# Kernel optimization log

Measured on AMD Instinct MI355X. Metric: run time of the kernel, lower is better.

The kernel has to match this reference:

```python
import jax, jax.numpy as jnp
import numpy as np


def causal_fft_conv(v, h):
    # v: [B, L, D], h: [L, D]; causal (linear, not circular) conv via zero-padded FFT
    L = v.shape[1]
    n = 2 * L
    Vf = jnp.fft.rfft(v, n=n, axis=1)          # [B, n//2+1, D]
    Hf = jnp.fft.rfft(h, n=n, axis=0)          # [n//2+1, D]
    y = jnp.fft.irfft(Vf * Hf[None], n=n, axis=1)
    return y[:, :L].astype(v.dtype)


def setup_inputs() -> dict:
    key = jax.random.key(0)
    ks = jax.random.split(key, 5)
    B, L, D = 4, 4096, 1024
    scale = 1.0 / np.sqrt(D)
    x = jax.random.normal(ks[0], (B, L, D), dtype=jnp.float32)
    Wu = jax.random.normal(ks[1], (D, D), dtype=jnp.float32) * scale
    Wv = jax.random.normal(ks[2], (D, D), dtype=jnp.float32) * scale
    Wo = jax.random.normal(ks[3], (D, D), dtype=jnp.float32) * scale
    h_filter = jax.random.normal(ks[4], (L, D), dtype=jnp.float32) * 0.02
    bu = jnp.zeros((D,), jnp.float32)
    bv = jnp.zeros((D,), jnp.float32)
    bo = jnp.zeros((D,), jnp.float32)
    return {"x": x, "Wu": Wu, "bu": bu, "Wv": Wv, "bv": bv,
            "h_filter": h_filter, "Wo": Wo, "bo": bo}


def reference(x, Wu, bu, Wv, bv, h_filter, Wo, bo):
    L = x.shape[1]
    u = jnp.einsum('bld,de->ble', x, Wu) + bu
    v = jnp.einsum('bld,de->ble', x, Wv) + bv
    t = jnp.arange(L, dtype=x.dtype)
    decay = jnp.exp(-0.01 * t)[:, None]          # [L, 1]
    h = h_filter * decay                          # [L, D]
    v_conv = causal_fft_conv(v, h)                # [B, L, D]
    y = u * v_conv
    y = jnp.einsum('bld,de->ble', y, Wo) + bo
    return y
```

## Files before the change

### kernel.cpp

```cpp
#include <hip/hip_runtime.h>
#include <hip/hip_bf16.h>
#include <hip/hip_fp16.h>
#include <string.h>

typedef __hip_bfloat16 bf16;
typedef _Float16 f16;
typedef __attribute__((ext_vector_type(8))) short short8;
typedef __attribute__((ext_vector_type(4))) float floatx4;
typedef __attribute__((ext_vector_type(4))) unsigned int uintx4;

#define GLD16(gp, lp) __builtin_amdgcn_global_load_lds( \
    (__attribute__((address_space(1))) void*)(gp),      \
    (__attribute__((address_space(3))) void*)(lp), 16, 0, 0)

__device__ __forceinline__ unsigned short bf16_bits(float f) {
  bf16 h = (bf16)f;
  unsigned short s;
  memcpy(&s, &h, 2);
  return s;
}
__device__ __forceinline__ __half2 u2h2(unsigned u) {
  __half2 h;
  memcpy(&h, &u, 4);
  return h;
}

__global__ __launch_bounds__(256)
void cvtx_k(const float* __restrict__ x, char* __restrict__ outbase,
            size_t bstride) {
  size_t e = ((size_t)blockIdx.x * 256 + threadIdx.x) * 8;
  int b = (int)(e >> 22);
  size_t i = e & 4194303;
  const floatx4* s = (const floatx4*)(x + e);
  floatx4 a0 = s[0], a1 = s[1];
  union { uintx4 u4; unsigned short us[8]; } w;
  w.us[0] = bf16_bits(a0.x); w.us[1] = bf16_bits(a0.y);
  w.us[2] = bf16_bits(a0.z); w.us[3] = bf16_bits(a0.w);
  w.us[4] = bf16_bits(a1.x); w.us[5] = bf16_bits(a1.y);
  w.us[6] = bf16_bits(a1.z); w.us[7] = bf16_bits(a1.w);
  *(uintx4*)((bf16*)(outbase + (size_t)b * bstride) + i) = w.u4;
}

__global__ __launch_bounds__(256)
void transpose_k(const float* __restrict__ W0, const float* __restrict__ W1,
                 const float* __restrict__ W2, bf16* __restrict__ T0,
                 bf16* __restrict__ T1, bf16* __restrict__ T2) {
  __shared__ bf16 t[64][66];
  const float* S = blockIdx.z == 0 ? W0 : (blockIdx.z == 1 ? W1 : W2);
  bf16* Dst      = blockIdx.z == 0 ? T0 : (blockIdx.z == 1 ? T1 : T2);
  const int tx = threadIdx.x & 63, ty = threadIdx.x >> 6;
  const int kb = blockIdx.y * 64, nb = blockIdx.x * 64;
#pragma unroll
  for (int rr = 0; rr < 16; ++rr) {
    int r = ty * 16 + rr;
    t[r][tx] = (bf16)S[(size_t)(kb + r) * 1024 + nb + tx];
  }
  __syncthreads();
#pragma unroll
  for (int rr = 0; rr < 16; ++rr) {
    int r = ty * 16 + rr;
    Dst[(size_t)(nb + r) * 1024 + kb + tx] = t[tx][r];
  }
}

__global__ __launch_bounds__(256)
void hprep_k(const float* __restrict__ hf, f16* __restrict__ hp) {
  int idx = blockIdx.x * 256 + threadIdx.x;
  int dblk = idx >> 15;
  int rem = idx & 32767;
  int k = rem >> 6, dd = rem & 63;
  int d = dblk * 64 + dd;
  float val = hf[(size_t)k * 1024 + d] * __expf(-0.01f * (float)k);
  hp[idx] = (f16)val;
}

__device__ __forceinline__
void gemm_body256(const bf16* __restrict__ A, const bf16* __restrict__ Bt,
                  const float* __restrict__ bias, void* __restrict__ Cout,
                  int out_mode, int m0, int n0) {
  constexpr int K = 1024;
  __shared__ __align__(16) bf16 Asl[2][16384];
  __shared__ __align__(16) bf16 Bsl[2][16384];
  const int tid = threadIdx.x;
  const int lane = tid & 63;
  const int wave = tid >> 6;
  const int wm = wave >> 2, wn = wave & 3;
  const int r = lane & 15, qlane = lane >> 4;

  floatx4 acc[8][4] = {};

  const bf16* gA[4];
  const bf16* gB[4];
#pragma unroll
  for (int is = 0; is < 4; ++is) {
    int p = is * 512 + tid;
    int m = p >> 3;
    int qe = (p & 7) ^ (m & 7);
    gA[is] = A  + (size_t)(m0 + m) * K + qe * 8;
    gB[is] = Bt + (size_t)(n0 + m) * K + qe * 8;
  }
  const int wbyte = wave * 1024;

  const int rx = r & 7;
  const int aRow = (wm * 128 + r) * 128;
  const int bRow = (wn * 64 + r) * 128;
  const int a0off = aRow + ((qlane) ^ rx) * 16;
  const int a1off = aRow + ((4 + qlane) ^ rx) * 16;
  const int b0off = bRow + ((qlane) ^ rx) * 16;
  const int b1off = bRow + ((4 + qlane) ^ rx) * 16;

#pragma unroll
  for (int is = 0; is < 4; ++is)
    GLD16(gA[is], (char*)&Asl[0][0] + is * 8192 + wbyte);
#pragma unroll
  for (int is = 0; is < 4; ++is)
    GLD16(gB[is], (char*)&Bsl[0][0] + is * 8192 + wbyte);

  for (int kt = 0; kt < 16; ++kt) {
    const int cur = kt & 1;
    const char* Ab = (const char*)&Asl[cur][0];
    const char* Bb = (const char*)&Bsl[cur][0];

    if (kt < 15) {
      const int k0 = (kt + 1) * 64;
#pragma unroll
      for (int is = 0; is < 4; ++is)
        GLD16(gA[is] + k0, (char*)&Asl[cur ^ 1][0] + is * 8192 + wbyte);
#pragma unroll
      for (int is = 0; is < 4; ++is)
        GLD16(gB[is] + k0, (char*)&Bsl[cur ^ 1][0] + is * 8192 + wbyte);
      asm volatile("s_waitcnt vmcnt(8)" ::: "memory");
    } else {
      asm volatile("s_waitcnt vmcnt(0)" ::: "memory");
    }
    __builtin_amdgcn_s_barrier();

    {
      short8 af[8], bfr[4];
#pragma unroll
      for (int i = 0; i < 8; ++i)
        af[i] = *(const short8*)(Ab + a0off + i * 2048);
#pragma unroll
      for (int j = 0; j < 4; ++j)
        bfr[j] = *(const short8*)(Bb + b0off + j * 2048);
      __builtin_amdgcn_s_setprio(1);
#pragma unroll
      for (int i = 0; i < 8; ++i)
#pragma unroll
        for (int j = 0; j < 4; ++j)
          acc[i][j] = __builtin_amdgcn_mfma_f32_16x16x32_bf16(
              af[i], bfr[j], acc[i][j], 0, 0, 0);
      __builtin_amdgcn_s_setprio(0);
    }
    {
      short8 af[8], bfr[4];
#pragma unroll
      for (int i = 0; i < 8; ++i)
        af[i] = *(const short8*)(Ab + a1off + i * 2048);
#pragma unroll
      for (int j = 0; j < 4; ++j)
        bfr[j] = *(const short8*)(Bb + b1off + j * 2048);
      __builtin_amdgcn_s_setprio(1);
#pragma unroll
      for (int i = 0; i < 8; ++i)
#pragma unroll
        for (int j = 0; j < 4; ++j)
          acc[i][j] = __builtin_amdgcn_mfma_f32_16x16x32_bf16(
              af[i], bfr[j], acc[i][j], 0, 0, 0);
      __builtin_amdgcn_s_setprio(0);
    }
    __builtin_amdgcn_s_barrier();
  }

  const int cb = n0 + wn * 64;
  float bvv[4];
#pragma unroll
  for (int j = 0; j < 4; ++j) bvv[j] = bias[cb + j * 16 + r];
#pragma unroll
  for (int i = 0; i < 8; ++i) {
    int rowb = m0 + wm * 128 + i * 16 + qlane * 4;
#pragma unroll
    for (int j = 0; j < 4; ++j) {
      int col = cb + j * 16 + r;
#pragma unroll
      for (int v = 0; v < 4; ++v) {
        float val = acc[i][j][v] + bvv[j];
        size_t off = (size_t)(rowb + v) * 1024 + col;
        if (out_mode == 0)      ((bf16*)Cout)[off] = (bf16)val;
        else if (out_mode == 1) ((f16*)Cout)[off] = (f16)val;
        else                    ((float*)Cout)[off] = val;
      }
    }
  }
}

__global__ __launch_bounds__(512, 2)
void gemm_uv_k(const bf16* __restrict__ A, const bf16* __restrict__ WuT,
               const bf16* __restrict__ WvT, const float* __restrict__ bu,
               const float* __restrict__ bv, bf16* __restrict__ u_out,
               f16* __restrict__ v_out) {
  const int isv = blockIdx.z;
  gemm_body256(A, isv ? WvT : WuT, isv ? bv : bu,
               isv ? (void*)v_out : (void*)u_out, isv,
               blockIdx.x * 256, blockIdx.y * 256);
}

__global__ __launch_bounds__(512, 2)
void gemm_o_k(const bf16* __restrict__ A, const bf16* __restrict__ Bt,
              const float* __restrict__ bias, float* __restrict__ C) {
  gemm_body256(A, Bt, bias, (void*)C, 2, blockIdx.x * 256, blockIdx.y * 256);
}

__global__ __launch_bounds__(256)
void conv_k(const f16* __restrict__ vg0, const f16* __restrict__ hp,
            bf16* __restrict__ up0) {
  constexpr int CC = 64, TT = 128, D = 1024;
  __shared__ __align__(16) unsigned vs2[(TT + CC) * 32];
  __shared__ __align__(16) unsigned hs2[CC * 32];
  const int tid = threadIdx.x;
  const int pp = tid & 31, tg = tid >> 5;
  const int bx = blockIdx.x;
  const int t0 = blockIdx.y * TT;
  const int base = tg * 16;
  const unsigned* vg32 = (const unsigned*)(vg0 + (size_t)blockIdx.z * 4096 * D);
  unsigned* up32 = (unsigned*)(up0 + (size_t)blockIdx.z * 4096 * D);
  const uintx4* vg4 = (const uintx4*)vg32;
  const uintx4* hp4 = (const uintx4*)hp + (size_t)bx * 512 * 8;

  float ax[16], ay[16];
#pragma unroll
  for (int i = 0; i < 16; ++i) { ax[i] = 0.f; ay[i] = 0.f; }

  for (int c = 0; c < 8; ++c) {
    const int k0 = c * CC;
    __syncthreads();
    {
      uintx4* hd = (uintx4*)hs2;
      hd[tid] = hp4[k0 * 8 + tid];
      hd[tid + 256] = hp4[k0 * 8 + tid + 256];
    }
    {
      uintx4* vd = (uintx4*)vs2;
#pragma unroll
      for (int it = 0; it < 6; ++it) {
        int q = it * 256 + tid;
        int row = q >> 3, dp4 = q & 7;
        int tau = t0 - k0 - CC + row;
        uintx4 val = {0, 0, 0, 0};
        if (tau >= 0) val = vg4[(size_t)tau * 128 + bx * 8 + dp4];
        vd[q] = val;
      }
    }
    __syncthreads();

    __half2 p[16];
#pragma unroll
    for (int i = 0; i < 16; ++i)
      p[i] = u2h2(vs2[(base + i + CC) * 32 + pp]);
    __half2 acc2[16];
    const __half2 z2 = __float2half2_rn(0.f);
#pragma unroll
    for (int i = 0; i < 16; ++i) acc2[i] = z2;

    for (int kb = 0; kb < 4; ++kb) {
#pragma unroll
      for (int k2 = 0; k2 < 16; ++k2) {
        const int kk = kb * 16 + k2;
        __half2 hk = u2h2(hs2[kk * 32 + pp]);
#pragma unroll
        for (int i = 0; i < 16; ++i)
          acc2[i] = __hfma2(hk, p[(i - k2) & 15], acc2[i]);
        p[(15 - k2) & 15] = u2h2(vs2[(base + CC - 1 - kk) * 32 + pp]);
      }
    }
#pragma unroll
    for (int i = 0; i < 16; ++i) {
      ax[i] += __low2float(acc2[i]);
      ay[i] += __high2float(acc2[i]);
    }
  }

  const size_t rb = (size_t)(t0 + base) * 512 + bx * 32 + pp;
#pragma unroll
  for (int i = 0; i < 16; ++i) {
    unsigned uw = up32[rb + (size_t)i * 512];
    float ul = __uint_as_float((uw & 0xffffu) << 16);
    float uh = __uint_as_float(uw & 0xffff0000u);
    unsigned lo = bf16_bits(ul * ax[i]);
    unsigned hi = bf16_bits(uh * ay[i]);
    up32[rb + (size_t)i * 512] = lo | (hi << 16);
  }
}

extern "C" void kernel_launch(void* const* d_in, const int* in_sizes, int n_in,
                              void* d_out, int out_size, void* d_ws,
                              size_t ws_size, hipStream_t stream) {
  const float* x  = (const float*)d_in[0];
  const float* Wu = (const float*)d_in[1];
  const float* bu = (const float*)d_in[2];
  const float* Wv = (const float*)d_in[3];
  const float* bv = (const float*)d_in[4];
  const float* hf = (const float*)d_in[5];
  const float* Wo = (const float*)d_in[6];
  const float* bo = (const float*)d_in[7];
  char* ws = (char*)d_ws;
  bf16* WuT = (bf16*)(ws);
  bf16* WvT = (bf16*)(ws + 2097152);
  bf16* WoT = (bf16*)(ws + 4194304);
  f16*  hp  = (f16*)(ws + 6291456);

  dim3 tb(256);
  dim3 tg(512);
  transpose_k<<<dim3(16, 16, 3), tb, 0, stream>>>(Wu, Wv, Wo, WuT, WvT, WoT);
  hprep_k<<<dim3(2048), tb, 0, stream>>>(hf, hp);

  if (ws_size >= 42991616ull) {
    bf16* xb = (bf16*)d_out;
    f16*  vf = (f16*)((char*)d_out + 33554432);
    bf16* u  = (bf16*)(ws + 8388608);
    cvtx_k<<<dim3(8192), tb, 0, stream>>>(x, (char*)d_out, 8388608);
    gemm_uv_k<<<dim3(64, 4, 2), tg, 0, stream>>>(xb, WuT, WvT, bu, bv, u, vf);
    conv_k<<<dim3(16, 32, 4), tb, 0, stream>>>(vf, hp, u);
    gemm_o_k<<<dim3(64, 4), tg, 0, stream>>>(u, WoT, bo, (float*)d_out);
  } else {
    bf16* u_b = (bf16*)(ws + 8388608);
    cvtx_k<<<dim3(8192), tb, 0, stream>>>(x, (char*)d_out, 16777216);
    for (int b = 0; b < 4; ++b) {
      char* quarter = (char*)d_out + (size_t)b * 16777216;
      bf16* xb = (bf16*)quarter;
      f16*  vb = (f16*)(quarter + 8388608);
      float* outb = (float*)d_out + (size_t)b * 4194304;
      gemm_uv_k<<<dim3(16, 4, 2), tg, 0, stream>>>(xb, WuT, WvT, bu, bv,
                                                   u_b, vb);
      conv_k<<<dim3(16, 32, 1), tb, 0, stream>>>(vb, hp, u_b);
      gemm_o_k<<<dim3(16, 4), tg, 0, stream>>>(u_b, WoT, bo, outb);
    }
  }
}
```

Before: 419.2 us.

## Split GEMM k-tile into four quadrant phases with staggered prefetch

Restructures the 256x256 bf16 GEMM main loop so each k-tile is computed in four quadrant sub-phases (A-half x B-half). Global-to-LDS loads for the next tile are issued in pieces between phases, with finer vmcnt waits and barriers. The LDS data layout is remapped so each piece lands in the quadrant it feeds. The aim is to overlap loads with MFMA work and cut register pressure from fragments, in exchange for more barriers and tricky wait-count bookkeeping.

Result: slower. 432.0 us (+3.1%).

```diff
diff --git a/kernel.cpp b/kernel.cpp
--- a/kernel.cpp
+++ b/kernel.cpp
@@ -86,89 +86,156 @@
   const int wave = tid >> 6;
   const int wm = wave >> 2, wn = wave & 3;
   const int r = lane & 15, qlane = lane >> 4;
+  const int rx = r & 7;
+  const int lrow = lane >> 3;
+  const int lq = (lane & 7) ^ lrow;
 
   floatx4 acc[8][4] = {};
 
-  const bf16* gA[4];
-  const bf16* gB[4];
-#pragma unroll
-  for (int is = 0; is < 4; ++is) {
-    int p = is * 512 + tid;
-    int m = p >> 3;
-    int qe = (p & 7) ^ (m & 7);
-    gA[is] = A  + (size_t)(m0 + m) * K + qe * 8;
-    gB[is] = Bt + (size_t)(n0 + m) * K + qe * 8;
-  }
-  const int wbyte = wave * 1024;
-
-  const int rx = r & 7;
-  const int aRow = (wm * 128 + r) * 128;
-  const int bRow = (wn * 64 + r) * 128;
-  const int a0off = aRow + ((qlane) ^ rx) * 16;
-  const int a1off = aRow + ((4 + qlane) ^ rx) * 16;
-  const int b0off = bRow + ((qlane) ^ rx) * 16;
-  const int b1off = bRow + ((4 + qlane) ^ rx) * 16;
-
-#pragma unroll
-  for (int is = 0; is < 4; ++is)
-    GLD16(gA[is], (char*)&Asl[0][0] + is * 8192 + wbyte);
-#pragma unroll
-  for (int is = 0; is < 4; ++is)
-    GLD16(gB[is], (char*)&Bsl[0][0] + is * 8192 + wbyte);
+  const int rho0 = wave * 16, rho1 = rho0 + 8;
+  const int a1g0 = rho0 + (rho0 & 64), a1g1 = rho1 + (rho1 & 64);
+  const int a2g0 = a1g0 + 64,          a2g1 = a1g1 + 64;
+  const int b1g0 = ((rho0 >> 5) << 6) + (rho0 & 31);
+  const int b1g1 = ((rho1 >> 5) << 6) + (rho1 & 31);
+  const int b2g0 = b1g0 + 32,          b2g1 = b1g1 + 32;
+
+  const bf16* Ag = A  + (size_t)m0 * K + lq * 8;
+  const bf16* Bg = Bt + (size_t)n0 * K + lq * 8;
+  const bf16* gA1a = Ag + (size_t)(a1g0 + lrow) * K;
+  const bf16* gA1b = Ag + (size_t)(a1g1 + lrow) * K;
+  const bf16* gA2a = Ag + (size_t)(a2g0 + lrow) * K;
+  const bf16* gA2b = Ag + (size_t)(a2g1 + lrow) * K;
+  const bf16* gB1a = Bg + (size_t)(b1g0 + lrow) * K;
+  const bf16* gB1b = Bg + (size_t)(b1g1 + lrow) * K;
+  const bf16* gB2a = Bg + (size_t)(b2g0 + lrow) * K;
+  const bf16* gB2b = Bg + (size_t)(b2g1 + lrow) * K;
+
+  const int col0 = (qlane ^ rx) * 16;
+  const int col1 = ((4 + qlane) ^ rx) * 16;
+
+  {
+    char* An = (char*)&Asl[0][0];
+    char* Bn = (char*)&Bsl[0][0];
+    GLD16(gA1a, An + a1g0 * 128);
+    GLD16(gA1b, An + a1g1 * 128);
+    GLD16(gA2a, An + a2g0 * 128);
+    GLD16(gA2b, An + a2g1 * 128);
+    GLD16(gB1a, Bn + b1g0 * 128);
+    GLD16(gB1b, Bn + b1g1 * 128);
+    GLD16(gB2a, Bn + b2g0 * 128);
+    GLD16(gB2b, Bn + b2g1 * 128);
+    asm volatile("s_waitcnt vmcnt(0)" ::: "memory");
+    __builtin_amdgcn_s_barrier();
+  }
 
   for (int kt = 0; kt < 16; ++kt) {
-    const int cur = kt & 1;
-    const char* Ab = (const char*)&Asl[cur][0];
-    const char* Bb = (const char*)&Bsl[cur][0];
+    const int s = kt & 1;
+    const char* Ab = (const char*)&Asl[s][0];
+    const char* Bb = (const char*)&Bsl[s][0];
+    char* An = (char*)&Asl[s ^ 1][0];
+    char* Bn = (char*)&Bsl[s ^ 1][0];
+    const int kb = (kt + 1) * 64;
+    const char* Aw0 = Ab + wm * 16384 + r * 128 + col0;
+    const char* Aw1 = Ab + wm * 16384 + r * 128 + col1;
+    const char* Bw0 = Bb + wn * 8192 + r * 128 + col0;
+    const char* Bw1 = Bb + wn * 8192 + r * 128 + col1;
+    short8 af[4][2], bf[2][2];
 
     if (kt < 15) {
-      const int k0 = (kt + 1) * 64;
-#pragma unroll
-      for (int is = 0; is < 4; ++is)
-        GLD16(gA[is] + k0, (char*)&Asl[cur ^ 1][0] + is * 8192 + wbyte);
-#pragma unroll
-      for (int is = 0; is < 4; ++is)
-        GLD16(gB[is] + k0, (char*)&Bsl[cur ^ 1][0] + is * 8192 + wbyte);
-      asm volatile("s_waitcnt vmcnt(8)" ::: "memory");
+      GLD16(gA1a + kb, An + a1g0 * 128);
+      GLD16(gA1b + kb, An + a1g1 * 128);
+      asm volatile("s_waitcnt vmcnt(4)" ::: "memory");
+    } else {
+      asm volatile("s_waitcnt vmcnt(2)" ::: "memory");
+    }
+    __builtin_amdgcn_s_barrier();
+#pragma unroll
+    for (int i = 0; i < 4; ++i) {
+      af[i][0] = *(const short8*)(Aw0 + i * 2048);
+      af[i][1] = *(const short8*)(Aw1 + i * 2048);
+    }
+#pragma unroll
+    for (int j = 0; j < 2; ++j) {
+      bf[j][0] = *(const short8*)(Bw0 + j * 2048);
+      bf[j][1] = *(const short8*)(Bw1 + j * 2048);
+    }
+    __builtin_amdgcn_s_setprio(1);
+#pragma unroll
+    for (int ks = 0; ks < 2; ++ks)
+#pragma unroll
+      for (int i = 0; i < 4; ++i)
+#pragma unroll
+        for (int j = 0; j < 2; ++j)
+          acc[i][j] = __builtin_amdgcn_mfma_f32_16x16x32_bf16(
+              af[i][ks], bf[j][ks], acc[i][j], 0, 0, 0);
+    __builtin_amdgcn_s_setprio(0);
+
+    if (kt < 15) {
+      GLD16(gA2a + kb, An + a2g0 * 128);
+      GLD16(gA2b + kb, An + a2g1 * 128);
+      asm volatile("s_waitcnt vmcnt(4)" ::: "memory");
     } else {
       asm volatile("s_waitcnt vmcnt(0)" ::: "memory");
     }
     __builtin_amdgcn_s_barrier();
-
-    {
-      short8 af[8], bfr[4];
-#pragma unroll
-      for (int i = 0; i < 8; ++i)
-        af[i] = *(const short8*)(Ab + a0off + i * 2048);
-#pragma unroll
-      for (int j = 0; j < 4; ++j)
-        bfr[j] = *(const short8*)(Bb + b0off + j * 2048);
-      __builtin_amdgcn_s_setprio(1);
-#pragma unroll
-      for (int i = 0; i < 8; ++i)
-#pragma unroll
-        for (int j = 0; j < 4; ++j)
-          acc[i][j] = __builtin_amdgcn_mfma_f32_16x16x32_bf16(
-              af[i], bfr[j], acc[i][j], 0, 0, 0);
-      __builtin_amdgcn_s_setprio(0);
-    }
-    {
-      short8 af[8], bfr[4];
-#pragma unroll
-      for (int i = 0; i < 8; ++i)
-        af[i] = *(const short8*)(Ab + a1off + i * 2048);
-#pragma unroll
-      for (int j = 0; j < 4; ++j)
-        bfr[j] = *(const short8*)(Bb + b1off + j * 2048);
-      __builtin_amdgcn_s_setprio(1);
-#pragma unroll
-      for (int i = 0; i < 8; ++i)
-#pragma unroll
-        for (int j = 0; j < 4; ++j)
-          acc[i][j] = __builtin_amdgcn_mfma_f32_16x16x32_bf16(
-              af[i], bfr[j], acc[i][j], 0, 0, 0);
-      __builtin_amdgcn_s_setprio(0);
-    }
+#pragma unroll
+    for (int j = 0; j < 2; ++j) {
+      bf[j][0] = *(const short8*)(Bw0 + (2 + j) * 2048);
+      bf[j][1] = *(const short8*)(Bw1 + (2 + j) * 2048);
+    }
+    __builtin_amdgcn_s_setprio(1);
+#pragma unroll
+    for (int ks = 0; ks < 2; ++ks)
+#pragma unroll
+      for (int i = 0; i < 4; ++i)
+#pragma unroll
+        for (int j = 0; j < 2; ++j)
+          acc[i][2 + j] = __builtin_amdgcn_mfma_f32_16x16x32_bf16(
+              af[i][ks], bf[j][ks], acc[i][2 + j], 0, 0, 0);
+    __builtin_amdgcn_s_setprio(0);
+
+    if (kt < 15) {
+      GLD16(gB1a + kb, Bn + b1g0 * 128);
+      GLD16(gB1b + kb, Bn + b1g1 * 128);
+      asm volatile("s_waitcnt vmcnt(10)" ::: "memory");
+    }
+    __builtin_amdgcn_s_barrier();
+#pragma unroll
+    for (int i = 0; i < 4; ++i) {
+      af[i][0] = *(const short8*)(Aw0 + 8192 + i * 2048);
+      af[i][1] = *(const short8*)(Aw1 + 8192 + i * 2048);
+    }
+    __builtin_amdgcn_s_setprio(1);
+#pragma unroll
+    for (int ks = 0; ks < 2; ++ks)
+#pragma unroll
+      for (int i = 0; i < 4; ++i)
+#pragma unroll
+        for (int j = 0; j < 2; ++j)
+          acc[4 + i][2 + j] = __builtin_amdgcn_mfma_f32_16x16x32_bf16(
+              af[i][ks], bf[j][ks], acc[4 + i][2 + j], 0, 0, 0);
+    __builtin_amdgcn_s_setprio(0);
+
+    if (kt < 15) {
+      GLD16(gB2a + kb, Bn + b2g0 * 128);
+      GLD16(gB2b + kb, Bn + b2g1 * 128);
+    }
+#pragma unroll
+    for (int j = 0; j < 2; ++j) {
+      bf[j][0] = *(const short8*)(Bw0 + j * 2048);
+      bf[j][1] = *(const short8*)(Bw1 + j * 2048);
+    }
+    __builtin_amdgcn_s_setprio(1);
+#pragma unroll
+    for (int ks = 0; ks < 2; ++ks)
+#pragma unroll
+      for (int i = 0; i < 4; ++i)
+#pragma unroll
+        for (int j = 0; j < 2; ++j)
+          acc[4 + i][j] = __builtin_amdgcn_mfma_f32_16x16x32_bf16(
+              af[i][ks], bf[j][ks], acc[4 + i][j], 0, 0, 0);
+    __builtin_amdgcn_s_setprio(0);
+    __builtin_amdgcn_sched_barrier(0);
     __builtin_amdgcn_s_barrier();
   }
 
```

## Restructure GEMM main loop into quadrant-pipelined 8-wave schedule with staggered prefetch

Applied to the files above, without the earlier changes.

The GEMM body now splits each K-tile into four quadrant sub-steps (A-half by B-half). Each sub-step interleaves its LDS fragment reads and half-tile global-to-LDS prefetches with MFMA bursts, separated by barriers and sched_barriers. The aim is to overlap memory traffic with matrix math and cut register pressure by holding only half the fragments at once. The conv loop also software-pipelines its filter-tap LDS loads two steps ahead. The trade-off is many more barriers per K-tile and tricky buffer-reuse ordering, which could stall or race.

New measurement: 438.8 us. 1.05x slower.

```diff
diff --git a/kernel.cpp b/kernel.cpp
--- a/kernel.cpp
+++ b/kernel.cpp
@@ -86,89 +86,168 @@
   const int wave = tid >> 6;
   const int wm = wave >> 2, wn = wave & 3;
   const int r = lane & 15, qlane = lane >> 4;
+  const int rx = r & 7;
+  const int lrow = lane >> 3;
+  const int lgr = (lane & 7) ^ lrow;
 
   floatx4 acc[8][4] = {};
 
-  const bf16* gA[4];
-  const bf16* gB[4];
-#pragma unroll
-  for (int is = 0; is < 4; ++is) {
-    int p = is * 512 + tid;
-    int m = p >> 3;
-    int qe = (p & 7) ^ (m & 7);
-    gA[is] = A  + (size_t)(m0 + m) * K + qe * 8;
-    gB[is] = Bt + (size_t)(n0 + m) * K + qe * 8;
-  }
-  const int wbyte = wave * 1024;
-
-  const int rx = r & 7;
-  const int aRow = (wm * 128 + r) * 128;
-  const int bRow = (wn * 64 + r) * 128;
-  const int a0off = aRow + ((qlane) ^ rx) * 16;
-  const int a1off = aRow + ((4 + qlane) ^ rx) * 16;
-  const int b0off = bRow + ((qlane) ^ rx) * 16;
-  const int b1off = bRow + ((4 + qlane) ^ rx) * 16;
-
-#pragma unroll
-  for (int is = 0; is < 4; ++is)
-    GLD16(gA[is], (char*)&Asl[0][0] + is * 8192 + wbyte);
-#pragma unroll
-  for (int is = 0; is < 4; ++is)
-    GLD16(gB[is], (char*)&Bsl[0][0] + is * 8192 + wbyte);
+  const int a1r0 = wave * 8 + lrow;
+  const int a1r1 = 128 + wave * 8 + lrow;
+  const int a2r0 = a1r0 + 64, a2r1 = a1r1 + 64;
+  const int bL0 = wave * 8 + lrow, bL1 = 64 + wave * 8 + lrow;
+  const int b1r0 = ((bL0 >> 5) << 6) + (bL0 & 31);
+  const int b1r1 = ((bL1 >> 5) << 6) + (bL1 & 31);
+  const int b2r0 = b1r0 + 32, b2r1 = b1r1 + 32;
+
+  const bf16* gA1a = A + (size_t)(m0 + a1r0) * K + lgr * 8;
+  const bf16* gA1b = A + (size_t)(m0 + a1r1) * K + lgr * 8;
+  const bf16* gA2a = A + (size_t)(m0 + a2r0) * K + lgr * 8;
+  const bf16* gA2b = A + (size_t)(m0 + a2r1) * K + lgr * 8;
+  const bf16* gB1a = Bt + (size_t)(n0 + b1r0) * K + lgr * 8;
+  const bf16* gB1b = Bt + (size_t)(n0 + b1r1) * K + lgr * 8;
+  const bf16* gB2a = Bt + (size_t)(n0 + b2r0) * K + lgr * 8;
+  const bf16* gB2b = Bt + (size_t)(n0 + b2r1) * K + lgr * 8;
+
+  const int dA1a = (wave * 8) * 128, dA1b = (128 + wave * 8) * 128;
+  const int dA2a = dA1a + 8192,      dA2b = dA1b + 8192;
+  const int bb0 = ((wave * 8) >> 5) * 64 + ((wave * 8) & 31);
+  const int bb1 = ((64 + wave * 8) >> 5) * 64 + ((64 + wave * 8) & 31);
+  const int dB1a = bb0 * 128, dB1b = bb1 * 128;
+  const int dB2a = dB1a + 4096, dB2b = dB1b + 4096;
+
+  {
+    char* A0 = (char*)&Asl[0][0];
+    char* B0 = (char*)&Bsl[0][0];
+    char* A1p = (char*)&Asl[1][0];
+    char* B1p = (char*)&Bsl[1][0];
+    GLD16(gA1a, A0 + dA1a); GLD16(gA1b, A0 + dA1b);
+    GLD16(gB1a, B0 + dB1a); GLD16(gB1b, B0 + dB1b);
+    GLD16(gB2a, B0 + dB2a); GLD16(gB2b, B0 + dB2b);
+    GLD16(gA2a, A0 + dA2a); GLD16(gA2b, A0 + dA2b);
+    GLD16(gA1a + 64, A1p + dA1a); GLD16(gA1b + 64, A1p + dA1b);
+    GLD16(gB2a + 64, B1p + dB2a); GLD16(gB2b + 64, B1p + dB2b);
+    GLD16(gA2a + 64, A1p + dA2a); GLD16(gA2b + 64, A1p + dA2b);
+    asm volatile("s_waitcnt vmcnt(6)" ::: "memory");
+    __builtin_amdgcn_s_barrier();
+  }
 
   for (int kt = 0; kt < 16; ++kt) {
-    const int cur = kt & 1;
-    const char* Ab = (const char*)&Asl[cur][0];
-    const char* Bb = (const char*)&Bsl[cur][0];
-
+    const int s = kt & 1;
+    const char* Ab = (const char*)&Asl[s][0];
+    const char* Bb = (const char*)&Bsl[s][0];
+    char* Ao = (char*)&Asl[s][0];
+    char* Bo = (char*)&Bsl[s][0];
+    char* Bn = (char*)&Bsl[s ^ 1][0];
+    const int k1 = (kt + 1) * 64, k2o = (kt + 2) * 64;
+    const char* Arow = Ab + (wm * 128 + r) * 128;
+    const char* Brow = Bb + (wn * 64 + r) * 128;
+    const int c0 = (qlane ^ rx) * 16, c1 = ((4 + qlane) ^ rx) * 16;
+    short8 af[4][2], bf[2][2];
+
+#pragma unroll
+    for (int mi = 0; mi < 4; ++mi) {
+      af[mi][0] = *(const short8*)(Arow + mi * 2048 + c0);
+      af[mi][1] = *(const short8*)(Arow + mi * 2048 + c1);
+    }
+#pragma unroll
+    for (int nj = 0; nj < 2; ++nj) {
+      bf[nj][0] = *(const short8*)(Brow + nj * 2048 + c0);
+      bf[nj][1] = *(const short8*)(Brow + nj * 2048 + c1);
+    }
     if (kt < 15) {
-      const int k0 = (kt + 1) * 64;
-#pragma unroll
-      for (int is = 0; is < 4; ++is)
-        GLD16(gA[is] + k0, (char*)&Asl[cur ^ 1][0] + is * 8192 + wbyte);
-#pragma unroll
-      for (int is = 0; is < 4; ++is)
-        GLD16(gB[is] + k0, (char*)&Bsl[cur ^ 1][0] + is * 8192 + wbyte);
-      asm volatile("s_waitcnt vmcnt(8)" ::: "memory");
+      GLD16(gB1a + k1, Bn + dB1a);
+      GLD16(gB1b + k1, Bn + dB1b);
+    }
+    asm volatile("s_waitcnt lgkmcnt(8)" ::: "memory");
+    __builtin_amdgcn_s_barrier();
+    asm volatile("s_waitcnt lgkmcnt(0)" ::: "memory");
+    __builtin_amdgcn_sched_barrier(0);
+    __builtin_amdgcn_s_setprio(1);
+#pragma unroll
+    for (int ks = 0; ks < 2; ++ks)
+#pragma unroll
+      for (int mi = 0; mi < 4; ++mi)
+#pragma unroll
+        for (int nj = 0; nj < 2; ++nj)
+          acc[mi][nj] = __builtin_amdgcn_mfma_f32_16x16x32_bf16(
+              af[mi][ks], bf[nj][ks], acc[mi][nj], 0, 0, 0);
+    __builtin_amdgcn_s_setprio(0);
+    __builtin_amdgcn_s_barrier();
+
+#pragma unroll
+    for (int nj = 0; nj < 2; ++nj) {
+      bf[nj][0] = *(const short8*)(Brow + 4096 + nj * 2048 + c0);
+      bf[nj][1] = *(const short8*)(Brow + 4096 + nj * 2048 + c1);
+    }
+    if (kt < 14) {
+      GLD16(gA1a + k2o, Ao + dA1a);
+      GLD16(gA1b + k2o, Ao + dA1b);
+    }
+    __builtin_amdgcn_s_barrier();
+    asm volatile("s_waitcnt lgkmcnt(0)" ::: "memory");
+    __builtin_amdgcn_sched_barrier(0);
+    __builtin_amdgcn_s_setprio(1);
+#pragma unroll
+    for (int ks = 0; ks < 2; ++ks)
+#pragma unroll
+      for (int mi = 0; mi < 4; ++mi)
+#pragma unroll
+        for (int nj = 0; nj < 2; ++nj)
+          acc[mi][2 + nj] = __builtin_amdgcn_mfma_f32_16x16x32_bf16(
+              af[mi][ks], bf[nj][ks], acc[mi][2 + nj], 0, 0, 0);
+    __builtin_amdgcn_s_setprio(0);
+    __builtin_amdgcn_s_barrier();
+
+#pragma unroll
+    for (int mi = 0; mi < 4; ++mi) {
+      af[mi][0] = *(const short8*)(Arow + 8192 + mi * 2048 + c0);
+      af[mi][1] = *(const short8*)(Arow + 8192 + mi * 2048 + c1);
+    }
+    if (kt < 14) {
+      GLD16(gB2a + k2o, Bo + dB2a);
+      GLD16(gB2b + k2o, Bo + dB2b);
+    }
+    __builtin_amdgcn_s_barrier();
+    asm volatile("s_waitcnt lgkmcnt(0)" ::: "memory");
+    __builtin_amdgcn_sched_barrier(0);
+    __builtin_amdgcn_s_setprio(1);
+#pragma unroll
+    for (int ks = 0; ks < 2; ++ks)
+#pragma unroll
+      for (int mi = 0; mi < 4; ++mi)
+#pragma unroll
+        for (int nj = 0; nj < 2; ++nj)
+          acc[4 + mi][2 + nj] = __builtin_amdgcn_mfma_f32_16x16x32_bf16(
+              af[mi][ks], bf[nj][ks], acc[4 + mi][2 + nj], 0, 0, 0);
+    __builtin_amdgcn_s_setprio(0);
+    __builtin_amdgcn_s_barrier();
+
+#pragma unroll
+    for (int nj = 0; nj < 2; ++nj) {
+      bf[nj][0] = *(const short8*)(Brow + nj * 2048 + c0);
+      bf[nj][1] = *(const short8*)(Brow + nj * 2048 + c1);
+    }
+    if (kt < 14) {
+      GLD16(gA2a + k2o, Ao + dA2a);
+      GLD16(gA2b + k2o, Ao + dA2b);
+      asm volatile("s_waitcnt vmcnt(6)" ::: "memory");
     } else {
       asm volatile("s_waitcnt vmcnt(0)" ::: "memory");
     }
     __builtin_amdgcn_s_barrier();
-
-    {
-      short8 af[8], bfr[4];
-#pragma unroll
-      for (int i = 0; i < 8; ++i)
-        af[i] = *(const short8*)(Ab + a0off + i * 2048);
-#pragma unroll
-      for (int j = 0; j < 4; ++j)
-        bfr[j] = *(const short8*)(Bb + b0off + j * 2048);
-      __builtin_amdgcn_s_setprio(1);
-#pragma unroll
-      for (int i = 0; i < 8; ++i)
-#pragma unroll
-        for (int j = 0; j < 4; ++j)
-          acc[i][j] = __builtin_amdgcn_mfma_f32_16x16x32_bf16(
-              af[i], bfr[j], acc[i][j], 0, 0, 0);
-      __builtin_amdgcn_s_setprio(0);
-    }
-    {
-      short8 af[8], bfr[4];
-#pragma unroll
-      for (int i = 0; i < 8; ++i)
-        af[i] = *(const short8*)(Ab + a1off + i * 2048);
-#pragma unroll
-      for (int j = 0; j < 4; ++j)
-        bfr[j] = *(const short8*)(Bb + b1off + j * 2048);
-      __builtin_amdgcn_s_setprio(1);
-#pragma unroll
-      for (int i = 0; i < 8; ++i)
-#pragma unroll
-        for (int j = 0; j < 4; ++j)
-          acc[i][j] = __builtin_amdgcn_mfma_f32_16x16x32_bf16(
-              af[i], bfr[j], acc[i][j], 0, 0, 0);
-      __builtin_amdgcn_s_setprio(0);
-    }
+    asm volatile("s_waitcnt lgkmcnt(0)" ::: "memory");
+    __builtin_amdgcn_sched_barrier(0);
+    __builtin_amdgcn_s_setprio(1);
+#pragma unroll
+    for (int ks = 0; ks < 2; ++ks)
+#pragma unroll
+      for (int mi = 0; mi < 4; ++mi)
+#pragma unroll
+        for (int nj = 0; nj < 2; ++nj)
+          acc[4 + mi][nj] = __builtin_amdgcn_mfma_f32_16x16x32_bf16(
+              af[mi][ks], bf[nj][ks], acc[4 + mi][nj], 0, 0, 0);
+    __builtin_amdgcn_s_setprio(0);
     __builtin_amdgcn_s_barrier();
   }
 
@@ -262,11 +341,15 @@
 #pragma unroll
     for (int i = 0; i < 16; ++i) acc2[i] = z2;
 
+    unsigned hb0 = hs2[pp];
+    unsigned hb1 = hs2[32 + pp];
     for (int kb = 0; kb < 4; ++kb) {
 #pragma unroll
       for (int k2 = 0; k2 < 16; ++k2) {
         const int kk = kb * 16 + k2;
-        __half2 hk = u2h2(hs2[kk * 32 + pp]);
+        __half2 hk = u2h2(hb0);
+        hb0 = hb1;
+        hb1 = hs2[((kk + 2) & 63) * 32 + pp];
 #pragma unroll
         for (int i = 0; i < 16; ++i)
           acc2[i] = __hfma2(hk, p[(i - k2) & 15], acc2[i]);
```
